# Kernel optimization log

Hardware: AMD Instinct MI355X
Metric: run time of the kernel (lower is better)

The kernel has to match this reference:

```python
import jax, jax.numpy as jnp
import numpy as np
from jax import lax

EPS = 1e-6
NUM_HEADS = 16
BSZ = 4


def _expected_alignment_train(p_choose):
    """p_choose: [B, T, S] -> alpha [B, T, S].
    q_ij = (1-p_{i,j-1}) q_{i,j-1} + a_{i-1,j};  a_ij = p_ij q_ij
    Per-step closed form: a_i = p_i * excl_cumprod(1-p_i) * cumsum(a_{i-1} / excl_cumprod_clamped)
    """
    B, T, S = p_choose.shape
    # safe exclusive cumprod of (1 - p) along src (fairseq exclusive_cumprod with eps clamp)
    one_minus_p = jnp.clip(1.0 - p_choose, EPS, 1.0)
    cp = jnp.cumprod(one_minus_p, axis=2)
    cumprod_1mp = jnp.concatenate([jnp.ones_like(cp[:, :, :1]), cp[:, :, :-1]], axis=2)
    cumprod_1mp_clamp = jnp.clip(cumprod_1mp, EPS, 1.0)

    init_attn = jnp.zeros((B, S), p_choose.dtype).at[:, 0].set(1.0)

    def step(prev_attn, xs):
        p_i, cp_i, cpc_i = xs  # each [B, S]
        alpha_i = jnp.clip(p_i * cp_i * jnp.cumsum(prev_attn / cpc_i, axis=1), 0.0, 1.0)
        return alpha_i, alpha_i

    xs = (jnp.swapaxes(p_choose, 0, 1),
          jnp.swapaxes(cumprod_1mp, 0, 1),
          jnp.swapaxes(cumprod_1mp_clamp, 0, 1))  # [T, B, S]
    _, alpha = lax.scan(step, init_attn, xs)
    alpha = jnp.swapaxes(alpha, 0, 1)  # [B, T, S]

    # mass preservation (no key padding): residual mass onto last source token
    residuals = 1.0 - jnp.clip(jnp.sum(alpha[:, :, :-1], axis=-1), 0.0, 1.0)
    alpha = alpha.at[:, :, -1].set(residuals)
    return alpha


def reference(q_proj, q_proj_dummy=None, *, _unused=None):
    raise NotImplementedError


def reference(q_proj, k_proj, v_proj, out_w, out_b, energy_bias):
    # q_proj/k_proj/v_proj: [bsz*num_heads, len, head_dim]
    energy = jnp.einsum('btd,bsd->bts', q_proj, k_proj) + energy_bias[0]
    p_choose = jax.nn.sigmoid(energy)                       # [B, T, S]
    alpha = _expected_alignment_train(p_choose)
    beta = alpha                                            # hard-aligned: expected_attention = alpha
    attn = jnp.einsum('bts,bsd->btd', beta, v_proj)         # [B, T, head_dim]
    BH, T, D = attn.shape
    attn = jnp.swapaxes(attn, 0, 1).reshape(T, BSZ, NUM_HEADS * D)  # [T, bsz, embed]
    out = attn @ out_w.T + out_b                            # out_proj
    return out, alpha


def setup_inputs():
    key = jax.random.key(0)
    ks = jax.random.split(key, 4)
    BH, T, S, D = 64, 1024, 1024, 64
    E = NUM_HEADS * D
    return {
        'q_proj': jax.random.normal(ks[0], (BH, T, D), jnp.float32) * 0.1,
        'k_proj': jax.random.normal(ks[1], (BH, S, D), jnp.float32) * 0.1,
        'v_proj': jax.random.normal(ks[2], (BH, S, D), jnp.float32),
        'out_w': jax.random.normal(ks[3], (E, E), jnp.float32) * 0.02,
        'out_b': jnp.zeros((E,), jnp.float32),
        'energy_bias': jnp.full((1,), -2.0, jnp.float32),
    }
```

## Files before the change

kernel.cpp:

```cpp
#include <hip/hip_runtime.h>

#define TT 1024
#define SSZ 1024
#define DD 64
#define BHN 64
#define BSZN 4
#define EEN 1024
#define EPSF 1e-6f

typedef float f32x4 __attribute__((ext_vector_type(4)));

__device__ float g_X[(size_t)TT * BSZN * EEN];

template<int CTRL, int RM>
__device__ __forceinline__ float f_dpp(float x, float ident) {
  return __builtin_bit_cast(float,
      __builtin_amdgcn_update_dpp(__builtin_bit_cast(int, ident),
                                  __builtin_bit_cast(int, x),
                                  CTRL, RM, 0xF, false));
}

__device__ __forceinline__ float wscan_add(float x) {
  x += f_dpp<0x111, 0xF>(x, 0.0f);
  x += f_dpp<0x112, 0xF>(x, 0.0f);
  x += f_dpp<0x114, 0xF>(x, 0.0f);
  x += f_dpp<0x118, 0xF>(x, 0.0f);
  x += f_dpp<0x142, 0xA>(x, 0.0f);
  x += f_dpp<0x143, 0xC>(x, 0.0f);
  return x;
}

__device__ __forceinline__ float wave_shr1(float x, float ident) {
  return f_dpp<0x138, 0xF>(x, ident);
}

__device__ __forceinline__ f32x4 aload(const float* p) {
  f32x4 r;
  asm volatile("global_load_dwordx4 %0, %1, off" : "=v"(r) : "v"(p));
  return r;
}
__device__ __forceinline__ void astore(float* p, f32x4 v) {
  asm volatile("global_store_dwordx4 %0, %1, off" :: "v"(p), "v"(v) : "memory");
}

__global__ __launch_bounds__(256) void k_energy(const float* __restrict__ Q,
                                                const float* __restrict__ Kp,
                                                const float* __restrict__ eb,
                                                float* __restrict__ P) {
  __shared__ float As[64][132];
  __shared__ float Bs[64][132];
  const int tid = threadIdx.x;
  const int b = blockIdx.x >> 6;
  const int tile = blockIdx.x & 63;
  const int m0 = (tile >> 3) << 7;
  const int n0 = (tile & 7) << 7;

  {
    const int kc = (tid & 15) << 2;
    const int rr = (tid >> 4) << 2;
    const float* qb = Q + (size_t)b * TT * DD;
    const float* kb = Kp + (size_t)b * SSZ * DD;
#pragma unroll
    for (int pass = 0; pass < 2; ++pass) {
      const int r = rr + (pass << 6);
      float4 a0 = *(const float4*)(qb + (size_t)(m0 + r + 0) * DD + kc);
      float4 a1 = *(const float4*)(qb + (size_t)(m0 + r + 1) * DD + kc);
      float4 a2 = *(const float4*)(qb + (size_t)(m0 + r + 2) * DD + kc);
      float4 a3 = *(const float4*)(qb + (size_t)(m0 + r + 3) * DD + kc);
      *(float4*)&As[kc + 0][r] = make_float4(a0.x, a1.x, a2.x, a3.x);
      *(float4*)&As[kc + 1][r] = make_float4(a0.y, a1.y, a2.y, a3.y);
      *(float4*)&As[kc + 2][r] = make_float4(a0.z, a1.z, a2.z, a3.z);
      *(float4*)&As[kc + 3][r] = make_float4(a0.w, a1.w, a2.w, a3.w);
      float4 b0 = *(const float4*)(kb + (size_t)(n0 + r + 0) * DD + kc);
      float4 b1 = *(const float4*)(kb + (size_t)(n0 + r + 1) * DD + kc);
      float4 b2 = *(const float4*)(kb + (size_t)(n0 + r + 2) * DD + kc);
      float4 b3 = *(const float4*)(kb + (size_t)(n0 + r + 3) * DD + kc);
      *(float4*)&Bs[kc + 0][r] = make_float4(b0.x, b1.x, b2.x, b3.x);
      *(float4*)&Bs[kc + 1][r] = make_float4(b0.y, b1.y, b2.y, b3.y);
      *(float4*)&Bs[kc + 2][r] = make_float4(b0.z, b1.z, b2.z, b3.z);
      *(float4*)&Bs[kc + 3][r] = make_float4(b0.w, b1.w, b2.w, b3.w);
    }
  }
  __syncthreads();

  const int tx = tid & 15, ty = tid >> 4;
  float acc[8][8];
#pragma unroll
  for (int i = 0; i < 8; ++i)
#pragma unroll
    for (int j = 0; j < 8; ++j) acc[i][j] = 0.0f;

#pragma unroll 8
  for (int k = 0; k < 64; ++k) {
    float4 a0 = *(const float4*)&As[k][ty << 3];
    float4 a1 = *(const float4*)&As[k][(ty << 3) + 4];
    float4 b0 = *(const float4*)&Bs[k][tx << 3];
    float4 b1 = *(const float4*)&Bs[k][(tx << 3) + 4];
    float av[8] = {a0.x, a0.y, a0.z, a0.w, a1.x, a1.y, a1.z, a1.w};
    float bv[8] = {b0.x, b0.y, b0.z, b0.w, b1.x, b1.y, b1.z, b1.w};
#pragma unroll
    for (int i = 0; i < 8; ++i)
#pragma unroll
      for (int j = 0; j < 8; ++j) acc[i][j] = fmaf(av[i], bv[j], acc[i][j]);
  }

  const float bias = eb[0];
#pragma unroll
  for (int i = 0; i < 8; ++i) {
    const size_t row = (size_t)b * TT + m0 + (ty << 3) + i;
    float o[8];
#pragma unroll
    for (int j = 0; j < 8; ++j) {
      float x = acc[i][j] + bias;
      o[j] = __builtin_amdgcn_rcpf(1.0f + __expf(-x));
    }
    float* dst = P + row * SSZ + n0 + (tx << 3);
    *(float4*)dst = make_float4(o[0], o[1], o[2], o[3]);
    *(float4*)(dst + 4) = make_float4(o[4], o[5], o[6], o[7]);
  }
}

#define STEP(T, QS) do {                                                       \
  const int t_ = (T);                                                          \
  asm volatile("s_waitcnt vmcnt(4)" ::: "memory");                             \
  __builtin_amdgcn_sched_barrier(0);                                           \
  float fn0 = 1.0f - QS.x, fn1 = 1.0f - QS.y, fn2 = 1.0f - QS.z, fn3 = 1.0f - QS.w; \
  { int rr = t_ + 5; if (rr > TT - 1) rr = TT - 1;                             \
    QS = aload(gq + (size_t)rr * SSZ); }                                       \
  float ln0 = fn0, ln1 = ln0 * fn1, ln2 = ln1 * fn2, ln3 = ln2 * fn3;          \
  float An0 = ln3;                                                             \
  float An1 = An0 * f_dpp<0x111, 0xF>(An0, 1.0f);                              \
  float An2 = An1 * f_dpp<0x112, 0xF>(An1, 1.0f);                              \
  float An3 = An2 * f_dpp<0x114, 0xF>(An2, 1.0f);                              \
  float An4 = An3 * f_dpp<0x118, 0xF>(An3, 1.0f);                              \
  float An5 = An4 * f_dpp<0x142, 0xA>(An4, 1.0f);                              \
  float An6 = An5 * f_dpp<0x143, 0xC>(An5, 1.0f);                              \
  float wEn = wave_shr1(An6, 1.0f);                                            \
  float bb0 = fminf(c0  * prev0, prev0);                                       \
  float bb1 = fminf(cl0 * prev1, prev1);                                       \
  float bb2 = fminf(cl1 * prev2, prev2);                                       \
  float bb3 = fminf(cl2 * prev3, prev3);                                       \
  float Blo1 = fmaf(fc0, bb0, bb1);                                            \
  float Blo2 = fmaf(fc1, Blo1, bb2);                                           \
  float Blo3 = fmaf(fc2, Blo2, bb3);                                           \
  float B_ = fc3 * Blo3;                                                       \
  B_ = fmaf(As0, f_dpp<0x111, 0xF>(B_, 0.0f), B_);                             \
  B_ = fmaf(As1, f_dpp<0x112, 0xF>(B_, 0.0f), B_);                             \
  B_ = fmaf(As2, f_dpp<0x114, 0xF>(B_, 0.0f), B_);                             \
  B_ = fmaf(As3, f_dpp<0x118, 0xF>(B_, 0.0f), B_);                             \
  B_ = fmaf(As4, f_dpp<0x142, 0xA>(B_, 0.0f), B_);                             \
  float Bfull = fmaf(As5, f_dpp<0x143, 0xC>(B_, 0.0f), B_);                    \
  float wB = wave_shr1(Bfull, 0.0f);                                           \
  if (lane == 63) ldsAB[t_ & 1][w] = make_float2(An6, Bfull);                  \
  asm volatile("s_waitcnt lgkmcnt(0)" ::: "memory");                           \
  __builtin_amdgcn_s_barrier();                                                \
  __builtin_amdgcn_sched_barrier(0);                                           \
  float2 ab0 = ldsAB[t_ & 1][0];                                               \
  float2 ab1 = ldsAB[t_ & 1][1];                                               \
  float2 ab2 = ldsAB[t_ & 1][2];                                               \
  float Ew = 0.0f;                                                             \
  if (w == 1) Ew = ab0.y;                                                      \
  else if (w == 2) Ew = fmaf(A1g, ab0.y, ab1.y);                               \
  else if (w == 3) Ew = fmaf(A2g, fmaf(A1g, ab0.y, ab1.y), ab2.y);             \
  float El = fmaf(wE, Ew, wB);                                                 \
  float D0 = bb0 + El;                                                         \
  float D1 = fmaf(lc0, El, Blo1);                                              \
  float D2 = fmaf(lc1, El, Blo2);                                              \
  float D3 = fmaf(lc2, El, Blo3);                                              \
  float a0 = fminf(fmaf(-fc0, D0, D0), 1.0f);                                  \
  float a1 = fminf(fmaf(-fc1, D1, D1), 1.0f);                                  \
  float a2 = fminf(fmaf(-fc2, D2, D2), 1.0f);                                  \
  float a3 = fminf(fmaf(-fc3, D3, D3), 1.0f);                                  \
  prev0 = a0; prev1 = a1; prev2 = a2; prev3 = a3;                              \
  f32x4 av4; av4.x = a0; av4.y = a1; av4.z = a2; av4.w = a3;                   \
  if (tid != 255) astore(gq + (size_t)t_ * SSZ, av4);                          \
  float la = (a0 + a1) + (a2 + a3);                                            \
  float wsum = wscan_add(la);                                                  \
  if (lane == 63 && w < 3) ldsS[t_ & 1][w] = wsum;                             \
  if (tid == 255) {                                                            \
    if (t_ > 0) {                                                              \
      float tot = ldsS[(t_ - 1) & 1][0] + ldsS[(t_ - 1) & 1][1]                \
                + ldsS[(t_ - 1) & 1][2] + wsum_prev;                           \
      float rest = tot - pend.w;                                               \
      pend.w = 1.0f - fminf(fmaxf(rest, 0.0f), 1.0f);                          \
      astore(gq + (size_t)(t_ - 1) * SSZ, pend);                               \
    }                                                                          \
    pend = av4; wsum_prev = wsum;                                              \
  }                                                                            \
  fc0 = fn0; fc1 = fn1; fc2 = fn2; fc3 = fn3;                                  \
  lc0 = ln0; lc1 = ln1; lc2 = ln2;                                             \
  As0 = An0; As1 = An1; As2 = An2; As3 = An3; As4 = An4; As5 = An5;            \
  wE = wEn;                                                                    \
  float Pw_ = 1.0f;                                                            \
  if (w > 0) Pw_ = ab0.x;                                                      \
  if (w > 1) Pw_ *= ab1.x;                                                     \
  if (w > 2) Pw_ *= ab2.x;                                                     \
  c0 = (Pw_ * 1e6f) * wEn;                                                     \
  cl0 = c0 * ln0; cl1 = c0 * ln1; cl2 = c0 * ln2;                              \
  A1g = ab1.x; A2g = ab2.x;                                                    \
} while (0)

__global__ __launch_bounds__(256, 1) void k_scan(float* __restrict__ A) {
  const int b = blockIdx.x;
  const int tid = threadIdx.x;
  const int w = tid >> 6;
  const int lane = tid & 63;
  __shared__ float2 ldsAB[2][4];
  __shared__ float ldsS[2][4];

  float* gq = A + (size_t)b * TT * SSZ + ((size_t)w << 8) + ((size_t)lane << 2);

  f32x4 q0 = aload(gq + (size_t)0 * SSZ);
  f32x4 q1 = aload(gq + (size_t)1 * SSZ);
  f32x4 q2 = aload(gq + (size_t)2 * SSZ);
  f32x4 q3 = aload(gq + (size_t)3 * SSZ);
  asm volatile("s_waitcnt vmcnt(0)" ::: "memory");
  __builtin_amdgcn_sched_barrier(0);

  float fc0 = 1.0f - q0.x, fc1 = 1.0f - q0.y, fc2 = 1.0f - q0.z, fc3 = 1.0f - q0.w;
  q0 = aload(gq + (size_t)4 * SSZ);
  float lc0 = fc0, lc1 = lc0 * fc1, lc2 = lc1 * fc2;
  float lc3 = lc2 * fc3;
  float As0 = lc3;
  float As1 = As0 * f_dpp<0x111, 0xF>(As0, 1.0f);
  float As2 = As1 * f_dpp<0x112, 0xF>(As1, 1.0f);
  float As3 = As2 * f_dpp<0x114, 0xF>(As2, 1.0f);
  float As4 = As3 * f_dpp<0x118, 0xF>(As3, 1.0f);
  float As5 = As4 * f_dpp<0x142, 0xA>(As4, 1.0f);
  float A6  = As5 * f_dpp<0x143, 0xC>(As5, 1.0f);
  float wE = wave_shr1(A6, 1.0f);
  if (lane == 63) ldsAB[1][w] = make_float2(A6, 0.0f);
  asm volatile("s_waitcnt lgkmcnt(0)" ::: "memory");
  __builtin_amdgcn_s_barrier();
  __builtin_amdgcn_sched_barrier(0);
  float2 pab0 = ldsAB[1][0], pab1 = ldsAB[1][1], pab2 = ldsAB[1][2];
  float A1g = pab1.x, A2g = pab2.x;
  float Pw = 1.0f;
  if (w > 0) Pw = pab0.x;
  if (w > 1) Pw *= pab1.x;
  if (w > 2) Pw *= pab2.x;
  float c0 = (Pw * 1e6f) * wE;
  float cl0 = c0 * lc0, cl1 = c0 * lc1, cl2 = c0 * lc2;

  float prev0 = (tid == 0) ? 1.0f : 0.0f;
  float prev1 = 0.0f, prev2 = 0.0f, prev3 = 0.0f;
  f32x4 pend; pend.x = 0.0f; pend.y = 0.0f; pend.z = 0.0f; pend.w = 0.0f;
  float wsum_prev = 0.0f;

  for (int t0 = 0; t0 < TT; t0 += 4) {
    STEP(t0 + 0, q1);
    STEP(t0 + 1, q2);
    STEP(t0 + 2, q3);
    STEP(t0 + 3, q0);
  }

  asm volatile("s_waitcnt lgkmcnt(0)" ::: "memory");
  __builtin_amdgcn_s_barrier();
  __builtin_amdgcn_sched_barrier(0);
  if (tid == 255) {
    float tot = ldsS[(TT - 1) & 1][0] + ldsS[(TT - 1) & 1][1]
              + ldsS[(TT - 1) & 1][2] + wsum_prev;
    float rest = tot - pend.w;
    pend.w = 1.0f - fminf(fmaxf(rest, 0.0f), 1.0f);
    astore(gq + (size_t)(TT - 1) * SSZ, pend);
  }
}

__global__ __launch_bounds__(256) void k_av(const float* __restrict__ Al,
                                            const float* __restrict__ V) {
  __shared__ float As[64][132];
  __shared__ float Bs[64][64];
  const int tid = threadIdx.x;
  const int bh = blockIdx.x >> 3;
  const int m0 = (blockIdx.x & 7) << 7;
  const int bz = bh >> 4, hh = bh & 15;
  const float* ab = Al + (size_t)bh * TT * SSZ;
  const float* vb = V + (size_t)bh * SSZ * DD;
  const int tx = tid & 15, ty = tid >> 4;

  float acc[8][4];
#pragma unroll
  for (int i = 0; i < 8; ++i)
#pragma unroll
    for (int j = 0; j < 4; ++j) acc[i][j] = 0.0f;

  for (int s0 = 0; s0 < SSZ; s0 += 64) {
    {
      const int kc = (tid & 15) << 2;
      const int rr = (tid >> 4) << 2;
#pragma unroll
      for (int pass = 0; pass < 2; ++pass) {
        const int r = rr + (pass << 6);
        float4 a0 = *(const float4*)(ab + (size_t)(m0 + r + 0) * SSZ + s0 + kc);
        float4 a1 = *(const float4*)(ab + (size_t)(m0 + r + 1) * SSZ + s0 + kc);
        float4 a2 = *(const float4*)(ab + (size_t)(m0 + r + 2) * SSZ + s0 + kc);
        float4 a3 = *(const float4*)(ab + (size_t)(m0 + r + 3) * SSZ + s0 + kc);
        *(float4*)&As[kc + 0][r] = make_float4(a0.x, a1.x, a2.x, a3.x);
        *(float4*)&As[kc + 1][r] = make_float4(a0.y, a1.y, a2.y, a3.y);
        *(float4*)&As[kc + 2][r] = make_float4(a0.z, a1.z, a2.z, a3.z);
        *(float4*)&As[kc + 3][r] = make_float4(a0.w, a1.w, a2.w, a3.w);
      }
#pragma unroll
      for (int pass = 0; pass < 4; ++pass) {
        const int vr = (tid >> 4) + (pass << 4);
        const int vc = (tid & 15) << 2;
        *(float4*)&Bs[vr][vc] = *(const float4*)(vb + (size_t)(s0 + vr) * DD + vc);
      }
    }
    __syncthreads();
#pragma unroll 8
    for (int k = 0; k < 64; ++k) {
      float4 a0 = *(const float4*)&As[k][ty << 3];
      float4 a1 = *(const float4*)&As[k][(ty << 3) + 4];
      float4 b0 = *(const float4*)&Bs[k][tx << 2];
      float av[8] = {a0.x, a0.y, a0.z, a0.w, a1.x, a1.y, a1.z, a1.w};
      float bv[4] = {b0.x, b0.y, b0.z, b0.w};
#pragma unroll
      for (int i = 0; i < 8; ++i)
#pragma unroll
        for (int j = 0; j < 4; ++j) acc[i][j] = fmaf(av[i], bv[j], acc[i][j]);
    }
    __syncthreads();
  }
#pragma unroll
  for (int i = 0; i < 8; ++i) {
    const int t = m0 + (ty << 3) + i;
    float* dst = g_X + ((size_t)t * BSZN + bz) * EEN + hh * DD + (tx << 2);
    *(float4*)dst = make_float4(acc[i][0], acc[i][1], acc[i][2], acc[i][3]);
  }
}

__global__ __launch_bounds__(256) void k_out(const float* __restrict__ W,
                                             const float* __restrict__ Bb,
                                             float* __restrict__ Out) {
  __shared__ float As[32][132];
  __shared__ float Bs[32][132];
  const int tid = threadIdx.x;
  const int m0 = (blockIdx.x >> 3) << 7;
  const int n0 = (blockIdx.x & 7) << 7;
  const int tx = tid & 15, ty = tid >> 4;
  const int kc = (tid & 7) << 2;
  const int r = (tid >> 3) << 2;

  float acc[8][8];
#pragma unroll
  for (int i = 0; i < 8; ++i)
#pragma unroll
    for (int j = 0; j < 8; ++j) acc[i][j] = 0.0f;

  for (int k0 = 0; k0 < EEN; k0 += 32) {
    {
      float4 x0 = *(const float4*)(g_X + (size_t)(m0 + r + 0) * EEN + k0 + kc);
      float4 x1 = *(const float4*)(g_X + (size_t)(m0 + r + 1) * EEN + k0 + kc);
      float4 x2 = *(const float4*)(g_X + (size_t)(m0 + r + 2) * EEN + k0 + kc);
      float4 x3 = *(const float4*)(g_X + (size_t)(m0 + r + 3) * EEN + k0 + kc);
      *(float4*)&As[kc + 0][r] = make_float4(x0.x, x1.x, x2.x, x3.x);
      *(float4*)&As[kc + 1][r] = make_float4(x0.y, x1.y, x2.y, x3.y);
      *(float4*)&As[kc + 2][r] = make_float4(x0.z, x1.z, x2.z, x3.z);
      *(float4*)&As[kc + 3][r] = make_float4(x0.w, x1.w, x2.w, x3.w);
      float4 w0 = *(const float4*)(W + (size_t)(n0 + r + 0) * EEN + k0 + kc);
      float4 w1 = *(const float4*)(W + (size_t)(n0 + r + 1) * EEN + k0 + kc);
      float4 w2 = *(const float4*)(W + (size_t)(n0 + r + 2) * EEN + k0 + kc);
      float4 w3 = *(const float4*)(W + (size_t)(n0 + r + 3) * EEN + k0 + kc);
      *(float4*)&Bs[kc + 0][r] = make_float4(w0.x, w1.x, w2.x, w3.x);
      *(float4*)&Bs[kc + 1][r] = make_float4(w0.y, w1.y, w2.y, w3.y);
      *(float4*)&Bs[kc + 2][r] = make_float4(w0.z, w1.z, w2.z, w3.z);
      *(float4*)&Bs[kc + 3][r] = make_float4(w0.w, w1.w, w2.w, w3.w);
    }
    __syncthreads();
#pragma unroll 8
    for (int k = 0; k < 32; ++k) {
      float4 a0 = *(const float4*)&As[k][ty << 3];
      float4 a1 = *(const float4*)&As[k][(ty << 3) + 4];
      float4 b0 = *(const float4*)&Bs[k][tx << 3];
      float4 b1 = *(const float4*)&Bs[k][(tx << 3) + 4];
      float av[8] = {a0.x, a0.y, a0.z, a0.w, a1.x, a1.y, a1.z, a1.w};
      float bv[8] = {b0.x, b0.y, b0.z, b0.w, b1.x, b1.y, b1.z, b1.w};
#pragma unroll
      for (int i = 0; i < 8; ++i)
#pragma unroll
        for (int j = 0; j < 8; ++j) acc[i][j] = fmaf(av[i], bv[j], acc[i][j]);
    }
    __syncthreads();
  }

  float4 bb0 = *(const float4*)(Bb + n0 + (tx << 3));
  float4 bb1 = *(const float4*)(Bb + n0 + (tx << 3) + 4);
  float bv[8] = {bb0.x, bb0.y, bb0.z, bb0.w, bb1.x, bb1.y, bb1.z, bb1.w};
#pragma unroll
  for (int i = 0; i < 8; ++i) {
    float o[8];
#pragma unroll
    for (int j = 0; j < 8; ++j) o[j] = acc[i][j] + bv[j];
    float* dst = Out + (size_t)(m0 + (ty << 3) + i) * EEN + n0 + (tx << 3);
    *(float4*)dst = make_float4(o[0], o[1], o[2], o[3]);
    *(float4*)(dst + 4) = make_float4(o[4], o[5], o[6], o[7]);
  }
}

extern "C" void kernel_launch(void* const* d_in, const int* in_sizes, int n_in,
                              void* d_out, int out_size, void* d_ws, size_t ws_size,
                              hipStream_t stream) {
  const float* Q  = (const float*)d_in[0];
  const float* K  = (const float*)d_in[1];
  const float* V  = (const float*)d_in[2];
  const float* W  = (const float*)d_in[3];
  const float* Bb = (const float*)d_in[4];
  const float* eb = (const float*)d_in[5];
  float* Out = (float*)d_out;
  float* Alpha = Out + (size_t)TT * BSZN * EEN;

  k_energy<<<dim3(BHN * 64), dim3(256), 0, stream>>>(Q, K, eb, Alpha);
  k_scan<<<dim3(BHN), dim3(256), 0, stream>>>(Alpha);
  k_av<<<dim3(BHN * 8), dim3(256), 0, stream>>>(Alpha, V);
  k_out<<<dim3(256), dim3(256), 0, stream>>>(W, Bb, Out);
}
```

Before: 819.3 us.

## Use bf16 MFMA for energy, AV and output projection GEMMs

Replaces the scalar FP32 FMA GEMMs for QK^T energy, alpha·V and the output projection with bf16 MFMA 16x16x32 kernels. Adds prep kernels that convert W to bf16 and transpose V to bf16. The scan emits a bf16 copy of alpha alongside the FP32 output for the AV GEMM. This trades FP32 accuracy in the energy and attention products for matrix-core throughput, and adds extra stores in the scan.

```diff
diff --git a/kernel.cpp b/kernel.cpp
--- a/kernel.cpp
+++ b/kernel.cpp
@@ -8,9 +8,15 @@
 #define EEN 1024
 #define EPSF 1e-6f
 
-typedef float f32x4 __attribute__((ext_vector_type(4)));
-
-__device__ float g_X[(size_t)TT * BSZN * EEN];
+using f32x4 = __attribute__((ext_vector_type(4))) float;
+using i32x2 = __attribute__((ext_vector_type(2))) int;
+using i32x4 = __attribute__((ext_vector_type(4))) int;
+using s16x8 = __attribute__((ext_vector_type(8))) short;
+
+__device__ unsigned short g_Pb[(size_t)BHN * TT * SSZ];
+__device__ unsigned short g_Vt[(size_t)BHN * DD * SSZ];
+__device__ unsigned short g_Wb[(size_t)EEN * EEN];
+__device__ unsigned short g_Xb[(size_t)TT * BSZN * EEN];
 
 template<int CTRL, int RM>
 __device__ __forceinline__ float f_dpp(float x, float ident) {
@@ -42,87 +48,119 @@
 __device__ __forceinline__ void astore(float* p, f32x4 v) {
   asm volatile("global_store_dwordx4 %0, %1, off" :: "v"(p), "v"(v) : "memory");
 }
+__device__ __forceinline__ void astore2(unsigned short* p, i32x2 v) {
+  asm volatile("global_store_dwordx2 %0, %1, off" :: "v"(p), "v"(v) : "memory");
+}
+
+__device__ __forceinline__ int cvt_pk(float lo, float hi) {
+  int r;
+  asm("v_cvt_pk_bf16_f32 %0, %1, %2" : "=v"(r) : "v"(lo), "v"(hi));
+  return r;
+}
+__device__ __forceinline__ unsigned short bfr(float x) {
+  unsigned u = __builtin_bit_cast(unsigned, x);
+  u += 0x7fffu + ((u >> 16) & 1u);
+  return (unsigned short)(u >> 16);
+}
+__device__ __forceinline__ s16x8 pack8p(const float* p) {
+  f32x4 a = *(const f32x4*)p;
+  f32x4 b = *(const f32x4*)(p + 4);
+  i32x4 r;
+  r[0] = cvt_pk(a[0], a[1]); r[1] = cvt_pk(a[2], a[3]);
+  r[2] = cvt_pk(b[0], b[1]); r[3] = cvt_pk(b[2], b[3]);
+  return __builtin_bit_cast(s16x8, r);
+}
+__device__ __forceinline__ s16x8 pack8f(float v0, float v1, float v2, float v3,
+                                        float v4, float v5, float v6, float v7) {
+  i32x4 r;
+  r[0] = cvt_pk(v0, v1); r[1] = cvt_pk(v2, v3);
+  r[2] = cvt_pk(v4, v5); r[3] = cvt_pk(v6, v7);
+  return __builtin_bit_cast(s16x8, r);
+}
+
+__global__ __launch_bounds__(256) void k_prep_w(const float* __restrict__ W) {
+  const size_t idx = ((size_t)blockIdx.x * 256 + threadIdx.x) * 8;
+  *(s16x8*)(g_Wb + idx) = pack8p(W + idx);
+}
+
+__global__ __launch_bounds__(256) void k_prep_v(const float* __restrict__ V) {
+  __shared__ float tile[64][65];
+  const int tid = threadIdx.x;
+  const int bh = blockIdx.x >> 4;
+  const int s0 = (blockIdx.x & 15) << 6;
+  {
+    const int r = tid >> 2, cq = (tid & 3) << 4;
+    const float* src = V + ((size_t)bh * SSZ + s0 + r) * DD + cq;
+    *(float4*)&tile[r][cq + 0]  = *(const float4*)(src + 0);
+    *(float4*)&tile[r][cq + 4]  = *(const float4*)(src + 4);
+    *(float4*)&tile[r][cq + 8]  = *(const float4*)(src + 8);
+    *(float4*)&tile[r][cq + 12] = *(const float4*)(src + 12);
+  }
+  __syncthreads();
+  {
+    const int d = tid >> 2, sq = (tid & 3) << 4;
+    unsigned short* dst = g_Vt + ((size_t)bh * DD + d) * SSZ + s0 + sq;
+    *(s16x8*)(dst + 0) = pack8f(tile[sq + 0][d], tile[sq + 1][d], tile[sq + 2][d], tile[sq + 3][d],
+                                tile[sq + 4][d], tile[sq + 5][d], tile[sq + 6][d], tile[sq + 7][d]);
+    *(s16x8*)(dst + 8) = pack8f(tile[sq + 8][d], tile[sq + 9][d], tile[sq + 10][d], tile[sq + 11][d],
+                                tile[sq + 12][d], tile[sq + 13][d], tile[sq + 14][d], tile[sq + 15][d]);
+  }
+}
 
 __global__ __launch_bounds__(256) void k_energy(const float* __restrict__ Q,
                                                 const float* __restrict__ Kp,
                                                 const float* __restrict__ eb,
                                                 float* __restrict__ P) {
-  __shared__ float As[64][132];
-  __shared__ float Bs[64][132];
-  const int tid = threadIdx.x;
-  const int b = blockIdx.x >> 6;
+  const int tid = threadIdx.x, w = tid >> 6, l = tid & 63;
+  const int rl = l & 15, kg = l >> 4;
+  const int bh = blockIdx.x >> 6;
   const int tile = blockIdx.x & 63;
-  const int m0 = (tile >> 3) << 7;
-  const int n0 = (tile & 7) << 7;
-
-  {
-    const int kc = (tid & 15) << 2;
-    const int rr = (tid >> 4) << 2;
-    const float* qb = Q + (size_t)b * TT * DD;
-    const float* kb = Kp + (size_t)b * SSZ * DD;
-#pragma unroll
-    for (int pass = 0; pass < 2; ++pass) {
-      const int r = rr + (pass << 6);
-      float4 a0 = *(const float4*)(qb + (size_t)(m0 + r + 0) * DD + kc);
-      float4 a1 = *(const float4*)(qb + (size_t)(m0 + r + 1) * DD + kc);
-      float4 a2 = *(const float4*)(qb + (size_t)(m0 + r + 2) * DD + kc);
-      float4 a3 = *(const float4*)(qb + (size_t)(m0 + r + 3) * DD + kc);
-      *(float4*)&As[kc + 0][r] = make_float4(a0.x, a1.x, a2.x, a3.x);
-      *(float4*)&As[kc + 1][r] = make_float4(a0.y, a1.y, a2.y, a3.y);
-      *(float4*)&As[kc + 2][r] = make_float4(a0.z, a1.z, a2.z, a3.z);
-      *(float4*)&As[kc + 3][r] = make_float4(a0.w, a1.w, a2.w, a3.w);
-      float4 b0 = *(const float4*)(kb + (size_t)(n0 + r + 0) * DD + kc);
-      float4 b1 = *(const float4*)(kb + (size_t)(n0 + r + 1) * DD + kc);
-      float4 b2 = *(const float4*)(kb + (size_t)(n0 + r + 2) * DD + kc);
-      float4 b3 = *(const float4*)(kb + (size_t)(n0 + r + 3) * DD + kc);
-      *(float4*)&Bs[kc + 0][r] = make_float4(b0.x, b1.x, b2.x, b3.x);
-      *(float4*)&Bs[kc + 1][r] = make_float4(b0.y, b1.y, b2.y, b3.y);
-      *(float4*)&Bs[kc + 2][r] = make_float4(b0.z, b1.z, b2.z, b3.z);
-      *(float4*)&Bs[kc + 3][r] = make_float4(b0.w, b1.w, b2.w, b3.w);
+  const int m0 = (tile >> 2) << 6;
+  const int n0 = (((tile & 3) << 2) + w) << 6;
+  const float* qb = Q + (size_t)bh * TT * DD;
+  const float* kb = Kp + (size_t)bh * SSZ * DD;
+
+  f32x4 acc[4][4];
+#pragma unroll
+  for (int i = 0; i < 4; ++i)
+#pragma unroll
+    for (int j = 0; j < 4; ++j) acc[i][j] = (f32x4)0.0f;
+
+#pragma unroll
+  for (int ks = 0; ks < 2; ++ks) {
+    const int kof = (ks << 5) + (kg << 3);
+    s16x8 af[4], bf[4];
+#pragma unroll
+    for (int fi = 0; fi < 4; ++fi)
+      af[fi] = pack8p(qb + (size_t)(m0 + fi * 16 + rl) * DD + kof);
+#pragma unroll
+    for (int fj = 0; fj < 4; ++fj)
+      bf[fj] = pack8p(kb + (size_t)(n0 + fj * 16 + rl) * DD + kof);
+#pragma unroll
+    for (int fi = 0; fi < 4; ++fi)
+#pragma unroll
+      for (int fj = 0; fj < 4; ++fj)
+        acc[fi][fj] = __builtin_amdgcn_mfma_f32_16x16x32_bf16(af[fi], bf[fj], acc[fi][fj], 0, 0, 0);
+  }
+
+  const float bias = eb[0];
+  float* pb = P + (size_t)bh * TT * SSZ;
+#pragma unroll
+  for (int fi = 0; fi < 4; ++fi)
+#pragma unroll
+    for (int r = 0; r < 4; ++r) {
+      const size_t rowoff = (size_t)(m0 + fi * 16 + (kg << 2) + r) * SSZ;
+#pragma unroll
+      for (int fj = 0; fj < 4; ++fj) {
+        float x = acc[fi][fj][r] + bias;
+        pb[rowoff + n0 + fj * 16 + rl] = __builtin_amdgcn_rcpf(1.0f + __expf(-x));
+      }
     }
-  }
-  __syncthreads();
-
-  const int tx = tid & 15, ty = tid >> 4;
-  float acc[8][8];
-#pragma unroll
-  for (int i = 0; i < 8; ++i)
-#pragma unroll
-    for (int j = 0; j < 8; ++j) acc[i][j] = 0.0f;
-
-#pragma unroll 8
-  for (int k = 0; k < 64; ++k) {
-    float4 a0 = *(const float4*)&As[k][ty << 3];
-    float4 a1 = *(const float4*)&As[k][(ty << 3) + 4];
-    float4 b0 = *(const float4*)&Bs[k][tx << 3];
-    float4 b1 = *(const float4*)&Bs[k][(tx << 3) + 4];
-    float av[8] = {a0.x, a0.y, a0.z, a0.w, a1.x, a1.y, a1.z, a1.w};
-    float bv[8] = {b0.x, b0.y, b0.z, b0.w, b1.x, b1.y, b1.z, b1.w};
-#pragma unroll
-    for (int i = 0; i < 8; ++i)
-#pragma unroll
-      for (int j = 0; j < 8; ++j) acc[i][j] = fmaf(av[i], bv[j], acc[i][j]);
-  }
-
-  const float bias = eb[0];
-#pragma unroll
-  for (int i = 0; i < 8; ++i) {
-    const size_t row = (size_t)b * TT + m0 + (ty << 3) + i;
-    float o[8];
-#pragma unroll
-    for (int j = 0; j < 8; ++j) {
-      float x = acc[i][j] + bias;
-      o[j] = __builtin_amdgcn_rcpf(1.0f + __expf(-x));
-    }
-    float* dst = P + row * SSZ + n0 + (tx << 3);
-    *(float4*)dst = make_float4(o[0], o[1], o[2], o[3]);
-    *(float4*)(dst + 4) = make_float4(o[4], o[5], o[6], o[7]);
-  }
 }
 
 #define STEP(T, QS) do {                                                       \
   const int t_ = (T);                                                          \
-  asm volatile("s_waitcnt vmcnt(4)" ::: "memory");                             \
+  asm volatile("s_waitcnt vmcnt(8)" ::: "memory");                             \
   __builtin_amdgcn_sched_barrier(0);                                           \
   float fn0 = 1.0f - QS.x, fn1 = 1.0f - QS.y, fn2 = 1.0f - QS.z, fn3 = 1.0f - QS.w; \
   { int rr = t_ + 5; if (rr > TT - 1) rr = TT - 1;                             \
@@ -173,7 +211,11 @@
   float a3 = fminf(fmaf(-fc3, D3, D3), 1.0f);                                  \
   prev0 = a0; prev1 = a1; prev2 = a2; prev3 = a3;                              \
   f32x4 av4; av4.x = a0; av4.y = a1; av4.z = a2; av4.w = a3;                   \
-  if (tid != 255) astore(gq + (size_t)t_ * SSZ, av4);                          \
+  if (tid != 255) {                                                            \
+    astore(gq + (size_t)t_ * SSZ, av4);                                        \
+    i32x2 pk; pk[0] = cvt_pk(a0, a1); pk[1] = cvt_pk(a2, a3);                  \
+    astore2(gpb + (size_t)t_ * SSZ, pk);                                       \
+  }                                                                            \
   float la = (a0 + a1) + (a2 + a3);                                            \
   float wsum = wscan_add(la);                                                  \
   if (lane == 63 && w < 3) ldsS[t_ & 1][w] = wsum;                             \
@@ -184,6 +226,8 @@
       float rest = tot - pend.w;                                               \
       pend.w = 1.0f - fminf(fmaxf(rest, 0.0f), 1.0f);                          \
       astore(gq + (size_t)(t_ - 1) * SSZ, pend);                               \
+      i32x2 pk2; pk2[0] = cvt_pk(pend.x, pend.y); pk2[1] = cvt_pk(pend.z, pend.w); \
+      astore2(gpb + (size_t)(t_ - 1) * SSZ, pk2);                              \
     }                                                                          \
     pend = av4; wsum_prev = wsum;                                              \
   }                                                                            \
@@ -209,6 +253,7 @@
   __shared__ float ldsS[2][4];
 
   float* gq = A + (size_t)b * TT * SSZ + ((size_t)w << 8) + ((size_t)lane << 2);
+  unsigned short* gpb = g_Pb + (size_t)b * TT * SSZ + ((size_t)w << 8) + ((size_t)lane << 2);
 
   f32x4 q0 = aload(gq + (size_t)0 * SSZ);
   f32x4 q1 = aload(gq + (size_t)1 * SSZ);
@@ -263,138 +308,79 @@
     float rest = tot - pend.w;
     pend.w = 1.0f - fminf(fmaxf(rest, 0.0f), 1.0f);
     astore(gq + (size_t)(TT - 1) * SSZ, pend);
-  }
-}
-
-__global__ __launch_bounds__(256) void k_av(const float* __restrict__ Al,
-                                            const float* __restrict__ V) {
-  __shared__ float As[64][132];
-  __shared__ float Bs[64][64];
-  const int tid = threadIdx.x;
-  const int bh = blockIdx.x >> 3;
-  const int m0 = (blockIdx.x & 7) << 7;
+    i32x2 pk; pk[0] = cvt_pk(pend.x, pend.y); pk[1] = cvt_pk(pend.z, pend.w);
+    astore2(gpb + (size_t)(TT - 1) * SSZ, pk);
+  }
+}
+
+__global__ __launch_bounds__(256) void k_av() {
+  const int tid = threadIdx.x, w = tid >> 6, l = tid & 63;
+  const int rl = l & 15, kg = l >> 4;
+  const int gw = blockIdx.x * 4 + w;
+  const int bh = gw >> 6;
+  const int t0 = (gw & 63) << 4;
+
+  const unsigned short* ab = g_Pb + ((size_t)bh * TT + t0 + rl) * SSZ;
+  const unsigned short* vb = g_Vt + (size_t)bh * DD * SSZ;
+
+  f32x4 acc[4];
+#pragma unroll
+  for (int j = 0; j < 4; ++j) acc[j] = (f32x4)0.0f;
+
+  for (int kk = 0; kk < 32; ++kk) {
+    const int kof = (kk << 5) + (kg << 3);
+    s16x8 a = *(const s16x8*)(ab + kof);
+#pragma unroll
+    for (int fj = 0; fj < 4; ++fj) {
+      s16x8 b = *(const s16x8*)(vb + (size_t)(fj * 16 + rl) * SSZ + kof);
+      acc[fj] = __builtin_amdgcn_mfma_f32_16x16x32_bf16(a, b, acc[fj], 0, 0, 0);
+    }
+  }
+
   const int bz = bh >> 4, hh = bh & 15;
-  const float* ab = Al + (size_t)bh * TT * SSZ;
-  const float* vb = V + (size_t)bh * SSZ * DD;
-  const int tx = tid & 15, ty = tid >> 4;
-
-  float acc[8][4];
-#pragma unroll
-  for (int i = 0; i < 8; ++i)
-#pragma unroll
-    for (int j = 0; j < 4; ++j) acc[i][j] = 0.0f;
-
-  for (int s0 = 0; s0 < SSZ; s0 += 64) {
-    {
-      const int kc = (tid & 15) << 2;
-      const int rr = (tid >> 4) << 2;
-#pragma unroll
-      for (int pass = 0; pass < 2; ++pass) {
-        const int r = rr + (pass << 6);
-        float4 a0 = *(const float4*)(ab + (size_t)(m0 + r + 0) * SSZ + s0 + kc);
-        float4 a1 = *(const float4*)(ab + (size_t)(m0 + r + 1) * SSZ + s0 + kc);
-        float4 a2 = *(const float4*)(ab + (size_t)(m0 + r + 2) * SSZ + s0 + kc);
-        float4 a3 = *(const float4*)(ab + (size_t)(m0 + r + 3) * SSZ + s0 + kc);
-        *(float4*)&As[kc + 0][r] = make_float4(a0.x, a1.x, a2.x, a3.x);
-        *(float4*)&As[kc + 1][r] = make_float4(a0.y, a1.y, a2.y, a3.y);
-        *(float4*)&As[kc + 2][r] = make_float4(a0.z, a1.z, a2.z, a3.z);
-        *(float4*)&As[kc + 3][r] = make_float4(a0.w, a1.w, a2.w, a3.w);
-      }
-#pragma unroll
-      for (int pass = 0; pass < 4; ++pass) {
-        const int vr = (tid >> 4) + (pass << 4);
-        const int vc = (tid & 15) << 2;
-        *(float4*)&Bs[vr][vc] = *(const float4*)(vb + (size_t)(s0 + vr) * DD + vc);
-      }
+#pragma unroll
+  for (int fj = 0; fj < 4; ++fj) {
+    const int d = fj * 16 + rl;
+#pragma unroll
+    for (int r = 0; r < 4; ++r) {
+      const int t = t0 + (kg << 2) + r;
+      g_Xb[((size_t)t * BSZN + bz) * EEN + hh * DD + d] = bfr(acc[fj][r]);
     }
-    __syncthreads();
-#pragma unroll 8
-    for (int k = 0; k < 64; ++k) {
-      float4 a0 = *(const float4*)&As[k][ty << 3];
-      float4 a1 = *(const float4*)&As[k][(ty << 3) + 4];
-      float4 b0 = *(const float4*)&Bs[k][tx << 2];
-      float av[8] = {a0.x, a0.y, a0.z, a0.w, a1.x, a1.y, a1.z, a1.w};
-      float bv[4] = {b0.x, b0.y, b0.z, b0.w};
-#pragma unroll
-      for (int i = 0; i < 8; ++i)
-#pragma unroll
-        for (int j = 0; j < 4; ++j) acc[i][j] = fmaf(av[i], bv[j], acc[i][j]);
+  }
+}
+
+__global__ __launch_bounds__(256) void k_out(const float* __restrict__ Bb,
+                                             float* __restrict__ Out) {
+  const int tid = threadIdx.x, w = tid >> 6, l = tid & 63;
+  const int rl = l & 15, kg = l >> 4;
+  const int gw = blockIdx.x * 4 + w;
+  const int m0 = (gw >> 4) << 4;
+  const int n0 = (gw & 15) << 6;
+
+  const unsigned short* xb = g_Xb + (size_t)(m0 + rl) * EEN;
+
+  f32x4 acc[4];
+#pragma unroll
+  for (int j = 0; j < 4; ++j) acc[j] = (f32x4)0.0f;
+
+  for (int kk = 0; kk < 32; ++kk) {
+    const int kof = (kk << 5) + (kg << 3);
+    s16x8 a = *(const s16x8*)(xb + kof);
+#pragma unroll
+    for (int fj = 0; fj < 4; ++fj) {
+      s16x8 b = *(const s16x8*)(g_Wb + (size_t)(n0 + fj * 16 + rl) * EEN + kof);
+      acc[fj] = __builtin_amdgcn_mfma_f32_16x16x32_bf16(a, b, acc[fj], 0, 0, 0);
     }
-    __syncthreads();
-  }
-#pragma unroll
-  for (int i = 0; i < 8; ++i) {
-    const int t = m0 + (ty << 3) + i;
-    float* dst = g_X + ((size_t)t * BSZN + bz) * EEN + hh * DD + (tx << 2);
-    *(float4*)dst = make_float4(acc[i][0], acc[i][1], acc[i][2], acc[i][3]);
-  }
-}
-
-__global__ __launch_bounds__(256) void k_out(const float* __restrict__ W,
-                                             const float* __restrict__ Bb,
-                                             float* __restrict__ Out) {
-  __shared__ float As[32][132];
-  __shared__ float Bs[32][132];
-  const int tid = threadIdx.x;
-  const int m0 = (blockIdx.x >> 3) << 7;
-  const int n0 = (blockIdx.x & 7) << 7;
-  const int tx = tid & 15, ty = tid >> 4;
-  const int kc = (tid & 7) << 2;
-  const int r = (tid >> 3) << 2;
-
-  float acc[8][8];
-#pragma unroll
-  for (int i = 0; i < 8; ++i)
-#pragma unroll
-    for (int j = 0; j < 8; ++j) acc[i][j] = 0.0f;
-
-  for (int k0 = 0; k0 < EEN; k0 += 32) {
-    {
-      float4 x0 = *(const float4*)(g_X + (size_t)(m0 + r + 0) * EEN + k0 + kc);
-      float4 x1 = *(const float4*)(g_X + (size_t)(m0 + r + 1) * EEN + k0 + kc);
-      float4 x2 = *(const float4*)(g_X + (size_t)(m0 + r + 2) * EEN + k0 + kc);
-      float4 x3 = *(const float4*)(g_X + (size_t)(m0 + r + 3) * EEN + k0 + kc);
-      *(float4*)&As[kc + 0][r] = make_float4(x0.x, x1.x, x2.x, x3.x);
-      *(float4*)&As[kc + 1][r] = make_float4(x0.y, x1.y, x2.y, x3.y);
-      *(float4*)&As[kc + 2][r] = make_float4(x0.z, x1.z, x2.z, x3.z);
-      *(float4*)&As[kc + 3][r] = make_float4(x0.w, x1.w, x2.w, x3.w);
-      float4 w0 = *(const float4*)(W + (size_t)(n0 + r + 0) * EEN + k0 + kc);
-      float4 w1 = *(const float4*)(W + (size_t)(n0 + r + 1) * EEN + k0 + kc);
-      float4 w2 = *(const float4*)(W + (size_t)(n0 + r + 2) * EEN + k0 + kc);
-      float4 w3 = *(const float4*)(W + (size_t)(n0 + r + 3) * EEN + k0 + kc);
-      *(float4*)&Bs[kc + 0][r] = make_float4(w0.x, w1.x, w2.x, w3.x);
-      *(float4*)&Bs[kc + 1][r] = make_float4(w0.y, w1.y, w2.y, w3.y);
-      *(float4*)&Bs[kc + 2][r] = make_float4(w0.z, w1.z, w2.z, w3.z);
-      *(float4*)&Bs[kc + 3][r] = make_float4(w0.w, w1.w, w2.w, w3.w);
+  }
+
+#pragma unroll
+  for (int fj = 0; fj < 4; ++fj) {
+    const float bias = Bb[n0 + fj * 16 + rl];
+#pragma unroll
+    for (int r = 0; r < 4; ++r) {
+      const int m = m0 + (kg << 2) + r;
+      Out[(size_t)m * EEN + n0 + fj * 16 + rl] = acc[fj][r] + bias;
     }
-    __syncthreads();
-#pragma unroll 8
-    for (int k = 0; k < 32; ++k) {
-      float4 a0 = *(const float4*)&As[k][ty << 3];
-      float4 a1 = *(const float4*)&As[k][(ty << 3) + 4];
-      float4 b0 = *(const float4*)&Bs[k][tx << 3];
-      float4 b1 = *(const float4*)&Bs[k][(tx << 3) + 4];
-      float av[8] = {a0.x, a0.y, a0.z, a0.w, a1.x, a1.y, a1.z, a1.w};
-      float bv[8] = {b0.x, b0.y, b0.z, b0.w, b1.x, b1.y, b1.z, b1.w};
-#pragma unroll
-      for (int i = 0; i < 8; ++i)
-#pragma unroll
-        for (int j = 0; j < 8; ++j) acc[i][j] = fmaf(av[i], bv[j], acc[i][j]);
-    }
-    __syncthreads();
-  }
-
-  float4 bb0 = *(const float4*)(Bb + n0 + (tx << 3));
-  float4 bb1 = *(const float4*)(Bb + n0 + (tx << 3) + 4);
-  float bv[8] = {bb0.x, bb0.y, bb0.z, bb0.w, bb1.x, bb1.y, bb1.z, bb1.w};
-#pragma unroll
-  for (int i = 0; i < 8; ++i) {
-    float o[8];
-#pragma unroll
-    for (int j = 0; j < 8; ++j) o[j] = acc[i][j] + bv[j];
-    float* dst = Out + (size_t)(m0 + (ty << 3) + i) * EEN + n0 + (tx << 3);
-    *(float4*)dst = make_float4(o[0], o[1], o[2], o[3]);
-    *(float4*)(dst + 4) = make_float4(o[4], o[5], o[6], o[7]);
   }
 }
 
@@ -410,8 +396,10 @@
   float* Out = (float*)d_out;
   float* Alpha = Out + (size_t)TT * BSZN * EEN;
 
+  k_prep_w<<<dim3(512), dim3(256), 0, stream>>>(W);
+  k_prep_v<<<dim3(BHN * 16), dim3(256), 0, stream>>>(V);
   k_energy<<<dim3(BHN * 64), dim3(256), 0, stream>>>(Q, K, eb, Alpha);
   k_scan<<<dim3(BHN), dim3(256), 0, stream>>>(Alpha);
-  k_av<<<dim3(BHN * 8), dim3(256), 0, stream>>>(Alpha, V);
-  k_out<<<dim3(256), dim3(256), 0, stream>>>(W, Bb, Out);
-}
+  k_av<<<dim3(1024), dim3(256), 0, stream>>>();
+  k_out<<<dim3(1024), dim3(256), 0, stream>>>(Bb, Out);
+}
```

Measured after the change: 779.3 us. 1.05x faster.
